# Kernel tuning notes

Measured on AMD Instinct MI355X. Metric: run time of the kernel, lower is better.

Reference implementation:

```python
import jax, jax.numpy as jnp
import numpy as np

EMBED_DIM = 768
NUM_HEADS = 8
HEAD_DIM = EMBED_DIM // NUM_HEADS
WINDOW_HALF = (17 - 1) // 2          # window_size=17 -> 8
GAP = 3 + 1                          # dilation_gap=3 -> stride 4
OVERLAP = WINDOW_HALF * GAP          # 32
N_LINES = 8192


def setup_inputs() -> dict:
    key = jax.random.key(0)
    k1, k2, k3, k4, k5 = jax.random.split(key, 5)
    D = EMBED_DIM
    return {
        "main": jax.random.normal(k1, (N_LINES, D), dtype=jnp.float32),
        "begin": jax.random.normal(k2, (OVERLAP, D), dtype=jnp.float32),
        "end": jax.random.normal(k3, (OVERLAP, D), dtype=jnp.float32),
        "in_proj_w": jax.random.normal(k4, (3 * D, D), dtype=jnp.float32) * 0.02,
        "in_proj_b": jnp.zeros((3 * D,), dtype=jnp.float32),
        "out_proj_w": jax.random.normal(k5, (D, D), dtype=jnp.float32) * 0.02,
        "out_proj_b": jnp.zeros((D,), dtype=jnp.float32),
    }


def reference(main, begin, end, in_proj_w, in_proj_b, out_proj_w, out_proj_b):
    N, D = main.shape
    H, hd = NUM_HEADS, HEAD_DIM
    # combined buffer [begin | main | end]; the per-token shifted concatenations
    # in the torch loop are equivalent to a strided gather into this buffer.
    combined = jnp.concatenate([begin, main, end], axis=0)  # [N + 2*OVERLAP, D]
    offsets = jnp.concatenate([
        jnp.arange(-OVERLAP, 0, GAP),
        jnp.arange(GAP, OVERLAP + GAP, GAP),
    ])  # [2*WINDOW_HALF] = [16]
    idx = jnp.arange(N)[:, None] + OVERLAP + offsets[None, :]  # [N, W]
    keys = combined[idx]  # [N, W, D] dilated window keys (= values)

    wq, wk, wv = in_proj_w[:D], in_proj_w[D:2 * D], in_proj_w[2 * D:]
    bq, bk, bv = in_proj_b[:D], in_proj_b[D:2 * D], in_proj_b[2 * D:]

    q = (main @ wq.T + bq).reshape(N, H, hd) * (hd ** -0.5)   # [N,H,hd]
    k = (keys @ wk.T + bk).reshape(N, -1, H, hd)              # [N,W,H,hd]
    v = (keys @ wv.T + bv).reshape(N, -1, H, hd)              # [N,W,H,hd]

    scores = jnp.einsum('nhd,nwhd->nhw', q, k)                # [N,H,W]
    attn = jax.nn.softmax(scores, axis=-1)
    ctx = jnp.einsum('nhw,nwhd->nhd', attn, v).reshape(N, D)
    attn_out = ctx @ out_proj_w.T + out_proj_b                # [N,D]
    return jnp.concatenate([main, attn_out], axis=-1)         # [N,2D]
```

## Files before the change

### kernel.cpp

```cpp
#include <hip/hip_runtime.h>
#include <math.h>

#define D 768
#define NQKV 2304
#define NH 8
#define HD 96
#define NW 16
#define OVL 32
#define NLINES 8192
#define NCOMB 8256
#define MPAD 8320
#define CH 64
#define SCALE_Q 0.1020620726159657f
#define COMB_BLOCKS 6240

typedef int i32x8 __attribute__((ext_vector_type(8)));
typedef float f32x4 __attribute__((ext_vector_type(4)));
typedef float f32x2 __attribute__((ext_vector_type(2)));

__device__ __forceinline__ unsigned int pk_fp8x4(float a, float b, float c, float d) {
    int u = __builtin_amdgcn_cvt_pk_fp8_f32(a, b, 0, false);
    u = __builtin_amdgcn_cvt_pk_fp8_f32(c, d, u, true);
    return (unsigned int)u;
}
__device__ __forceinline__ unsigned char f2fp8(float v) {
    return (unsigned char)(__builtin_amdgcn_cvt_pk_fp8_f32(v, v, 0, false) & 0xFF);
}
template <bool HI>
__device__ __forceinline__ f32x2 upk(unsigned int u) {
    return __builtin_amdgcn_cvt_pk_f32_fp8((int)u, HI);
}
__device__ __forceinline__ float dot4f8(unsigned int a, unsigned int b) {
    const f32x2 al = upk<false>(a), ah = upk<true>(a);
    const f32x2 bl = upk<false>(b), bh = upk<true>(b);
    return al.x * bl.x + al.y * bl.y + ah.x * bh.x + ah.y * bh.y;
}

__device__ __forceinline__ void stage16(const void* g, void* l) {
    __builtin_amdgcn_global_load_lds(
        (const __attribute__((address_space(1))) unsigned int*)g,
        (__attribute__((address_space(3))) unsigned int*)l, 16, 0, 0);
}

__device__ __forceinline__ void stage_sw(const unsigned char* gbase, unsigned char* lds, int ch) {
    const int row = ch >> 3;
    const int half = ch & 1;
    const int o = (((ch >> 1) & 3) - row) & 3;
    stage16(gbase + (size_t)row * D + o * 32 + half * 16, lds + ch * 16);
}

__global__ __launch_bounds__(256) void convert_all(const float* __restrict__ main_,
                                                   const float* __restrict__ begin_,
                                                   const float* __restrict__ end_,
                                                   const float* __restrict__ in_w,
                                                   const float* __restrict__ in_b,
                                                   const float* __restrict__ out_w,
                                                   unsigned int* __restrict__ comb_dst,
                                                   unsigned int* __restrict__ w_dst,
                                                   float* __restrict__ bias_s) {
    const int bid = blockIdx.x;
    if (bid < COMB_BLOCKS) {
        const int i = bid * 256 + threadIdx.x;
        const int row = i / 192, c4 = i % 192;
        float4 v = make_float4(0.f, 0.f, 0.f, 0.f);
        if (row < NCOMB) {
            const float* src = (row < OVL) ? begin_ + (size_t)row * D
                             : (row < OVL + NLINES) ? main_ + (size_t)(row - OVL) * D
                                                    : end_ + (size_t)(row - OVL - NLINES) * D;
            v = *(const float4*)(src + c4 * 4);
        }
        comb_dst[(size_t)row * 192 + c4] = pk_fp8x4(v.x, v.y, v.z, v.w);
    } else {
        const int j = (bid - COMB_BLOCKS) * 256 + threadIdx.x;
        const int f0 = j * 4;
        const bool is_out = f0 >= 3 * D * D;
        const float4 v = is_out ? *(const float4*)(out_w + (f0 - 3 * D * D))
                                : *(const float4*)(in_w + f0);
        const float s = 16.0f * ((f0 < D * D) ? SCALE_Q : 1.0f);
        w_dst[j] = pk_fp8x4(v.x * s, v.y * s, v.z * s, v.w * s);
        if (bid == COMB_BLOCKS) {
            for (int b = threadIdx.x; b < NQKV; b += 256)
                bias_s[b] = in_b[b] * (b < D ? SCALE_Q : 1.0f);
        }
    }
}

__global__ __launch_bounds__(256) void qkv_gemm(const unsigned char* __restrict__ comb,
                                                const unsigned char* __restrict__ w_f8,
                                                const float* __restrict__ bias_s,
                                                unsigned char* __restrict__ Qb,
                                                unsigned char* __restrict__ Kb,
                                                unsigned char* __restrict__ Vb) {
    __shared__ __align__(16) unsigned char As[128 * 128];
    __shared__ __align__(16) unsigned char Bs[128 * 128];
    const int bx = blockIdx.x;
    const int m0 = blockIdx.y * 128;
    const int n0 = bx * 128;
    const int tid = threadIdx.x;
    const int lane = tid & 63;
    const int wave = tid >> 6;
    const int wm = (wave & 1) * 64, wn = (wave >> 1) * 64;
    const int q = lane >> 4, l15 = lane & 15;
    const int swq = (q + l15) & 3;

    f32x4 acc[4][4] = {};
    for (int k0 = 0; k0 < D; k0 += 128) {
#pragma unroll
        for (int it = 0; it < 4; it++) {
            const int ch = tid + it * 256;
            stage_sw(comb + (size_t)m0 * D + k0, As, ch);
            stage_sw(w_f8 + (size_t)n0 * D + k0, Bs, ch);
        }
        __syncthreads();
        i32x8 af[4], bfr[4];
#pragma unroll
        for (int i = 0; i < 4; i++)
            af[i] = *(const i32x8*)(As + (wm + i * 16 + l15) * 128 + swq * 32);
#pragma unroll
        for (int j = 0; j < 4; j++)
            bfr[j] = *(const i32x8*)(Bs + (wn + j * 16 + l15) * 128 + swq * 32);
#pragma unroll
        for (int i = 0; i < 4; i++)
#pragma unroll
            for (int j = 0; j < 4; j++)
                acc[i][j] = __builtin_amdgcn_mfma_scale_f32_16x16x128_f8f6f4(
                    af[i], bfr[j], acc[i][j], 0, 0, 0, 127, 0, 123);
        __syncthreads();
    }

    unsigned char* Cb = (bx < 6) ? Qb : (bx < 12 ? Kb : Vb);
    const int nloc = (bx % 6) * 128;
#pragma unroll
    for (int i = 0; i < 4; i++)
#pragma unroll
        for (int j = 0; j < 4; j++)
#pragma unroll
            for (int r = 0; r < 4; r++) {
                const int row = m0 + wm + i * 16 + q * 4 + r;
                const int col = wn + j * 16 + l15;
                Cb[(size_t)row * D + nloc + col] = f2fp8(acc[i][j][r] + bias_s[bx * 128 + col]);
            }
}

__global__ __launch_bounds__(256) void out_gemm(const unsigned char* __restrict__ ctx,
                                                const unsigned char* __restrict__ w,
                                                const float* __restrict__ bias,
                                                const float* __restrict__ main_,
                                                float* __restrict__ out) {
    __shared__ __align__(16) unsigned char As[64 * 128];
    __shared__ __align__(16) unsigned char Bs[128 * 128];
    const int m0 = blockIdx.y * 64;
    const int n0 = blockIdx.x * 128;
    const int tid = threadIdx.x;
    const int lane = tid & 63;
    const int wave = tid >> 6;
    const int wn = wave * 32;
    const int q = lane >> 4, l15 = lane & 15;
    const int swq = (q + l15) & 3;

    f32x4 acc[4][2] = {};
    for (int k0 = 0; k0 < D; k0 += 128) {
#pragma unroll
        for (int it = 0; it < 2; it++)
            stage_sw(ctx + (size_t)m0 * D + k0, As, tid + it * 256);
#pragma unroll
        for (int it = 0; it < 4; it++)
            stage_sw(w + (size_t)n0 * D + k0, Bs, tid + it * 256);
        __syncthreads();
        i32x8 af[4], bfr[2];
#pragma unroll
        for (int i = 0; i < 4; i++)
            af[i] = *(const i32x8*)(As + (i * 16 + l15) * 128 + swq * 32);
#pragma unroll
        for (int j = 0; j < 2; j++)
            bfr[j] = *(const i32x8*)(Bs + (wn + j * 16 + l15) * 128 + swq * 32);
#pragma unroll
        for (int i = 0; i < 4; i++)
#pragma unroll
            for (int j = 0; j < 2; j++)
                acc[i][j] = __builtin_amdgcn_mfma_scale_f32_16x16x128_f8f6f4(
                    af[i], bfr[j], acc[i][j], 0, 0, 0, 127, 0, 123);
        __syncthreads();
    }

#pragma unroll
    for (int i = 0; i < 4; i++)
#pragma unroll
        for (int j = 0; j < 2; j++)
#pragma unroll
            for (int r = 0; r < 4; r++) {
                const int row = m0 + i * 16 + q * 4 + r;
                const int col = n0 + wn + j * 16 + l15;
                out[(size_t)row * (2 * D) + D + col] = acc[i][j][r] + bias[col];
            }
#pragma unroll
    for (int it = 0; it < 8; it++) {
        const int idx = tid + it * 256;
        const int r = idx >> 5, c4 = idx & 31;
        const float4 v = *(const float4*)(main_ + (size_t)(m0 + r) * D + n0 + c4 * 4);
        *(float4*)(out + (size_t)(m0 + r) * (2 * D) + n0 + c4 * 4) = v;
    }
}

__global__ __launch_bounds__(256) void attn_kernel(const unsigned char* __restrict__ Q,
                                                   const unsigned char* __restrict__ K,
                                                   const unsigned char* __restrict__ V,
                                                   unsigned char* __restrict__ ctx) {
    const int n0 = blockIdx.x * CH;
    const int h = blockIdx.y;
    const int tid = threadIdx.x;

    __shared__ __align__(16) unsigned char sK[128 * 128];
    __shared__ __align__(16) unsigned char sV[128 * 128];
    __shared__ float sS[CH][17];

    const int l = tid & 63;
    const int wg = tid >> 6;

#pragma unroll
    for (int it = 0; it < 3; it++) {
        const int idx = tid + it * 256;
        const int row = idx / 6, c = idx % 6;
        const int slot = (c + row) & 7;
        *(uint4*)(sK + row * 128 + slot * 16) =
            *(const uint4*)(K + (size_t)(n0 + row) * D + h * HD + c * 16);
        *(uint4*)(sV + row * 128 + slot * 16) =
            *(const uint4*)(V + (size_t)(n0 + row) * D + h * HD + c * 16);
    }
    uint4 qreg[6];
#pragma unroll
    for (int c = 0; c < 6; c++)
        qreg[c] = *(const uint4*)(Q + (size_t)(n0 + l) * D + h * HD + c * 16);
    __syncthreads();

#pragma unroll
    for (int wi = 0; wi < 4; wi++) {
        const int w = wg * 4 + wi;
        const int lrow = l + 4 * w + (w >= 8 ? 4 : 0);
        float s = 0.f;
#pragma unroll
        for (int c = 0; c < 6; c++) {
            const uint4 ka = *(const uint4*)(sK + lrow * 128 + ((c + lrow) & 7) * 16);
            s += dot4f8(qreg[c].x, ka.x) + dot4f8(qreg[c].y, ka.y) +
                 dot4f8(qreg[c].z, ka.z) + dot4f8(qreg[c].w, ka.w);
        }
        sS[l][w] = s;
    }
    __syncthreads();

    if (tid < CH) {
        float mx = -1e30f;
#pragma unroll
        for (int i = 0; i < NW; i++) mx = fmaxf(mx, sS[tid][i]);
        float e[NW], sum = 0.f;
#pragma unroll
        for (int i = 0; i < NW; i++) {
            e[i] = __expf(sS[tid][i] - mx);
            sum += e[i];
        }
        const float inv = 1.f / sum;
#pragma unroll
        for (int i = 0; i < NW; i++) sS[tid][i] = e[i] * inv;
    }
    __syncthreads();

    float p[NW];
#pragma unroll
    for (int i = 0; i < NW; i++) p[i] = sS[l][i];
    float acc[24] = {};
#pragma unroll
    for (int i = 0; i < NW; i++) {
        const int lrow = l + 4 * i + (i >= 8 ? 4 : 0);
        const unsigned char* vrow = sV + lrow * 128;
        const float pw = p[i];
#pragma unroll
        for (int c = 0; c < 3; c++) {
            const int off = wg * 24 + c * 8;
            const uint2 vv =
                *(const uint2*)(vrow + (((off >> 4) + lrow) & 7) * 16 + (off & 15));
            const f32x2 a0 = upk<false>(vv.x), a1 = upk<true>(vv.x);
            const f32x2 a2 = upk<false>(vv.y), a3 = upk<true>(vv.y);
            acc[c * 8 + 0] += pw * a0.x;
            acc[c * 8 + 1] += pw * a0.y;
            acc[c * 8 + 2] += pw * a1.x;
            acc[c * 8 + 3] += pw * a1.y;
            acc[c * 8 + 4] += pw * a2.x;
            acc[c * 8 + 5] += pw * a2.y;
            acc[c * 8 + 6] += pw * a3.x;
            acc[c * 8 + 7] += pw * a3.y;
        }
    }
    unsigned char* op = ctx + (size_t)(n0 + l) * D + h * HD + wg * 24;
#pragma unroll
    for (int c = 0; c < 3; c++) {
        const unsigned int u0 =
            pk_fp8x4(acc[c * 8 + 0], acc[c * 8 + 1], acc[c * 8 + 2], acc[c * 8 + 3]);
        const unsigned int u1 =
            pk_fp8x4(acc[c * 8 + 4], acc[c * 8 + 5], acc[c * 8 + 6], acc[c * 8 + 7]);
        *(uint2*)(op + c * 8) = make_uint2(u0, u1);
    }
}

extern "C" void kernel_launch(void* const* d_in, const int* in_sizes, int n_in,
                              void* d_out, int out_size, void* d_ws, size_t ws_size,
                              hipStream_t stream) {
    const float* main_ = (const float*)d_in[0];
    const float* begin_ = (const float*)d_in[1];
    const float* end_ = (const float*)d_in[2];
    const float* in_w = (const float*)d_in[3];
    const float* in_b = (const float*)d_in[4];
    const float* out_w = (const float*)d_in[5];
    const float* out_b = (const float*)d_in[6];
    float* out = (float*)d_out;

    unsigned char* comb_f8 = (unsigned char*)d_ws;
    unsigned char* w_f8 = comb_f8 + (size_t)MPAD * D;
    unsigned char* Qb = w_f8 + (size_t)4 * D * D;
    unsigned char* Kb = Qb + (size_t)MPAD * D;
    unsigned char* Vb = Kb + (size_t)MPAD * D;
    unsigned char* ctx_f8 = Vb + (size_t)MPAD * D;
    float* bias_s = (float*)(ctx_f8 + (size_t)NLINES * D);

    convert_all<<<COMB_BLOCKS + 4 * D * D / 1024, 256, 0, stream>>>(
        main_, begin_, end_, in_w, in_b, out_w, (unsigned int*)comb_f8,
        (unsigned int*)w_f8, bias_s);
    qkv_gemm<<<dim3(NQKV / 128, MPAD / 128), 256, 0, stream>>>(comb_f8, w_f8, bias_s,
                                                               Qb, Kb, Vb);
    attn_kernel<<<dim3(NLINES / CH, NH), 256, 0, stream>>>(Qb + (size_t)OVL * D, Kb, Vb,
                                                           ctx_f8);
    out_gemm<<<dim3(D / 128, NLINES / 64), 256, 0, stream>>>(ctx_f8, w_f8 + (size_t)3 * D * D,
                                                             out_b, main_, out);
}
```

Before: 171.0 us.

## Swizzle workgroup order across XCDs and move main passthrough copy into convert

Adds an XCD-aware remapping of the linear workgroup index in the QKV GEMM, attention and output GEMM kernels, so each XCD gets a contiguous range of tiles and neighbouring tiles share its L2. The copy of `main` into the left half of the output moves from out_gemm into convert_all, which already reads `main`, so a second global read of that data goes away. The risk is extra index arithmetic and a possibly worse tile-to-XCD mapping when the grid shapes change.

```diff
diff --git a/kernel.cpp b/kernel.cpp
--- a/kernel.cpp
+++ b/kernel.cpp
@@ -49,6 +49,12 @@
     stage16(gbase + (size_t)row * D + o * 32 + half * 16, lds + ch * 16);
 }
 
+__device__ __forceinline__ int xcd_swz(int lin, int nwg) {
+    const int q = nwg >> 3, r = nwg & 7;
+    const int x = lin & 7, i = lin >> 3;
+    return (x < r ? x * (q + 1) : r * (q + 1) + (x - r) * q) + i;
+}
+
 __global__ __launch_bounds__(256) void convert_all(const float* __restrict__ main_,
                                                    const float* __restrict__ begin_,
                                                    const float* __restrict__ end_,
@@ -57,7 +63,8 @@
                                                    const float* __restrict__ out_w,
                                                    unsigned int* __restrict__ comb_dst,
                                                    unsigned int* __restrict__ w_dst,
-                                                   float* __restrict__ bias_s) {
+                                                   float* __restrict__ bias_s,
+                                                   float* __restrict__ out) {
     const int bid = blockIdx.x;
     if (bid < COMB_BLOCKS) {
         const int i = bid * 256 + threadIdx.x;
@@ -68,6 +75,8 @@
                              : (row < OVL + NLINES) ? main_ + (size_t)(row - OVL) * D
                                                     : end_ + (size_t)(row - OVL - NLINES) * D;
             v = *(const float4*)(src + c4 * 4);
+            if (row >= OVL && row < OVL + NLINES)
+                *(float4*)(out + (size_t)(row - OVL) * (2 * D) + c4 * 4) = v;
         }
         comb_dst[(size_t)row * 192 + c4] = pk_fp8x4(v.x, v.y, v.z, v.w);
     } else {
@@ -93,8 +102,10 @@
                                                 unsigned char* __restrict__ Vb) {
     __shared__ __align__(16) unsigned char As[128 * 128];
     __shared__ __align__(16) unsigned char Bs[128 * 128];
-    const int bx = blockIdx.x;
-    const int m0 = blockIdx.y * 128;
+    const int lin = blockIdx.y * 18 + blockIdx.x;
+    const int s = xcd_swz(lin, 18 * 65);
+    const int bx = s % 18;
+    const int m0 = (s / 18) * 128;
     const int n0 = bx * 128;
     const int tid = threadIdx.x;
     const int lane = tid & 63;
@@ -145,12 +156,13 @@
 __global__ __launch_bounds__(256) void out_gemm(const unsigned char* __restrict__ ctx,
                                                 const unsigned char* __restrict__ w,
                                                 const float* __restrict__ bias,
-                                                const float* __restrict__ main_,
                                                 float* __restrict__ out) {
     __shared__ __align__(16) unsigned char As[64 * 128];
     __shared__ __align__(16) unsigned char Bs[128 * 128];
-    const int m0 = blockIdx.y * 64;
-    const int n0 = blockIdx.x * 128;
+    const int lin = blockIdx.y * 6 + blockIdx.x;
+    const int s = xcd_swz(lin, 6 * 128);
+    const int m0 = (s / 6) * 64;
+    const int n0 = (s % 6) * 128;
     const int tid = threadIdx.x;
     const int lane = tid & 63;
     const int wave = tid >> 6;
@@ -193,21 +205,16 @@
                 const int col = n0 + wn + j * 16 + l15;
                 out[(size_t)row * (2 * D) + D + col] = acc[i][j][r] + bias[col];
             }
-#pragma unroll
-    for (int it = 0; it < 8; it++) {
-        const int idx = tid + it * 256;
-        const int r = idx >> 5, c4 = idx & 31;
-        const float4 v = *(const float4*)(main_ + (size_t)(m0 + r) * D + n0 + c4 * 4);
-        *(float4*)(out + (size_t)(m0 + r) * (2 * D) + n0 + c4 * 4) = v;
-    }
 }
 
 __global__ __launch_bounds__(256) void attn_kernel(const unsigned char* __restrict__ Q,
                                                    const unsigned char* __restrict__ K,
                                                    const unsigned char* __restrict__ V,
                                                    unsigned char* __restrict__ ctx) {
-    const int n0 = blockIdx.x * CH;
-    const int h = blockIdx.y;
+    const int lin = blockIdx.y * 128 + blockIdx.x;
+    const int s = xcd_swz(lin, 128 * 8);
+    const int n0 = (s % 128) * CH;
+    const int h = s / 128;
     const int tid = threadIdx.x;
 
     __shared__ __align__(16) unsigned char sK[128 * 128];
@@ -237,14 +244,14 @@
     for (int wi = 0; wi < 4; wi++) {
         const int w = wg * 4 + wi;
         const int lrow = l + 4 * w + (w >= 8 ? 4 : 0);
-        float s = 0.f;
+        float sc = 0.f;
 #pragma unroll
         for (int c = 0; c < 6; c++) {
             const uint4 ka = *(const uint4*)(sK + lrow * 128 + ((c + lrow) & 7) * 16);
-            s += dot4f8(qreg[c].x, ka.x) + dot4f8(qreg[c].y, ka.y) +
-                 dot4f8(qreg[c].z, ka.z) + dot4f8(qreg[c].w, ka.w);
-        }
-        sS[l][w] = s;
+            sc += dot4f8(qreg[c].x, ka.x) + dot4f8(qreg[c].y, ka.y) +
+                  dot4f8(qreg[c].z, ka.z) + dot4f8(qreg[c].w, ka.w);
+        }
+        sS[l][w] = sc;
     }
     __syncthreads();
 
@@ -323,11 +330,9 @@
 
     convert_all<<<COMB_BLOCKS + 4 * D * D / 1024, 256, 0, stream>>>(
         main_, begin_, end_, in_w, in_b, out_w, (unsigned int*)comb_f8,
-        (unsigned int*)w_f8, bias_s);
-    qkv_gemm<<<dim3(NQKV / 128, MPAD / 128), 256, 0, stream>>>(comb_f8, w_f8, bias_s,
-                                                               Qb, Kb, Vb);
-    attn_kernel<<<dim3(NLINES / CH, NH), 256, 0, stream>>>(Qb + (size_t)OVL * D, Kb, Vb,
-                                                           ctx_f8);
-    out_gemm<<<dim3(D / 128, NLINES / 64), 256, 0, stream>>>(ctx_f8, w_f8 + (size_t)3 * D * D,
-                                                             out_b, main_, out);
-}
+        (unsigned int*)w_f8, bias_s, out);
+    qkv_gemm<<<dim3(18, 65), 256, 0, stream>>>(comb_f8, w_f8, bias_s, Qb, Kb, Vb);
+    attn_kernel<<<dim3(128, NH), 256, 0, stream>>>(Qb + (size_t)OVL * D, Kb, Vb, ctx_f8);
+    out_gemm<<<dim3(6, 128), 256, 0, stream>>>(ctx_f8, w_f8 + (size_t)3 * D * D,
+                                               out_b, out);
+}
```

New measurement: 165.4 us. 1.03x faster.
